# Optimization experiments

Measured on AMD Instinct MI355X. Metric: run time of the kernel, lower is better.

The kernel has to match this reference:

```python
import jax, jax.numpy as jnp
import numpy as np


def _lstm_dir(x, Wih, Whh, bih, bhh, reverse):
    # x: [B,T,D]; Wih: [4H,D]; Whh: [4H,H]; PyTorch gate order i,f,g,o
    if reverse:
        x = x[:, ::-1, :]
    H = Whh.shape[1]
    B = x.shape[0]
    # precompute input projection for all timesteps: [B,T,4H]
    xW = jnp.einsum('btd,gd->btg', x, Wih) + bih + bhh
    xW = jnp.swapaxes(xW, 0, 1)  # [T,B,4H]
    h0 = jnp.zeros((B, H), x.dtype)
    c0 = jnp.zeros((B, H), x.dtype)

    def step(carry, xt):
        h, c = carry
        g = xt + h @ Whh.T
        i, f, gg, o = jnp.split(g, 4, axis=-1)
        c = jax.nn.sigmoid(f) * c + jax.nn.sigmoid(i) * jnp.tanh(gg)
        h = jax.nn.sigmoid(o) * jnp.tanh(c)
        return (h, c), h

    _, ys = jax.lax.scan(step, (h0, c0), xW)
    ys = jnp.swapaxes(ys, 0, 1)  # [B,T,H]
    if reverse:
        ys = ys[:, ::-1, :]
    return ys


def _bilstm(x, Wih_f, Whh_f, bih_f, bhh_f, Wih_b, Whh_b, bih_b, bhh_b):
    yf = _lstm_dir(x, Wih_f, Whh_f, bih_f, bhh_f, False)
    yb = _lstm_dir(x, Wih_b, Whh_b, bih_b, bhh_b, True)
    return jnp.concatenate([yf, yb], axis=-1)


def setup_inputs() -> dict:
    key = jax.random.key(0)
    B, T, D = 1024, 512, 30
    H1, H2, DENSE, OUT = 96, 64, 32, 1
    ks = jax.random.split(key, 21)

    def U(k, shape, fan):
        bnd = 1.0 / np.sqrt(fan)
        return jax.random.uniform(k, shape, jnp.float32, -bnd, bnd)

    x = jax.random.normal(ks[0], (B, T, D), jnp.float32)
    inp = {'x': x}
    # layer 1 (input D -> H1), forward and backward directions
    inp['Wih1f'] = U(ks[1], (4 * H1, D), H1)
    inp['Whh1f'] = U(ks[2], (4 * H1, H1), H1)
    inp['bih1f'] = U(ks[3], (4 * H1,), H1)
    inp['bhh1f'] = U(ks[4], (4 * H1,), H1)
    inp['Wih1b'] = U(ks[5], (4 * H1, D), H1)
    inp['Whh1b'] = U(ks[6], (4 * H1, H1), H1)
    inp['bih1b'] = U(ks[7], (4 * H1,), H1)
    inp['bhh1b'] = U(ks[8], (4 * H1,), H1)
    # layer 2 (input 2*H1 -> H2)
    inp['Wih2f'] = U(ks[9], (4 * H2, 2 * H1), H2)
    inp['Whh2f'] = U(ks[10], (4 * H2, H2), H2)
    inp['bih2f'] = U(ks[11], (4 * H2,), H2)
    inp['bhh2f'] = U(ks[12], (4 * H2,), H2)
    inp['Wih2b'] = U(ks[13], (4 * H2, 2 * H1), H2)
    inp['Whh2b'] = U(ks[14], (4 * H2, H2), H2)
    inp['bih2b'] = U(ks[15], (4 * H2,), H2)
    inp['bhh2b'] = U(ks[16], (4 * H2,), H2)
    # dense head
    inp['W1'] = U(ks[17], (DENSE, 2 * H2), 2 * H2)
    inp['b1'] = U(ks[18], (DENSE,), 2 * H2)
    inp['W2'] = U(ks[19], (OUT, DENSE), DENSE)
    inp['b2'] = U(ks[20], (OUT,), DENSE)
    return inp


def reference(x, Wih1f, Whh1f, bih1f, bhh1f, Wih1b, Whh1b, bih1b, bhh1b,
              Wih2f, Whh2f, bih2f, bhh2f, Wih2b, Whh2b, bih2b, bhh2b,
              W1, b1, W2, b2):
    # dropout layers are identity in eval mode
    h1 = _bilstm(x, Wih1f, Whh1f, bih1f, bhh1f, Wih1b, Whh1b, bih1b, bhh1b)   # [B,T,192]
    h2 = _bilstm(h1, Wih2f, Whh2f, bih2f, bhh2f, Wih2b, Whh2b, bih2b, bhh2b)  # [B,T,128]
    last = h2[:, -1, :]                       # [B,128]
    d = jax.nn.relu(last @ W1.T + b1)         # [B,32]
    return d @ W2.T + b2                      # [B,1]
```

## Files before the change

kernel.cpp:

```cpp
#include <hip/hip_runtime.h>
#include <math.h>

#define B_  1024
#define T_  512
#define D_  30
#define H1_ 96
#define G1_ 384
#define H2_ 64
#define G2_ 256

__device__ float g_h1[(size_t)B_ * T_ * 192];
__device__ float g_h2f[(size_t)B_ * H2_];

__device__ __forceinline__ float fast_tanh(float v) {
  float a = fabsf(v);
  float e = __expf(-2.0f * a);
  float t = 1.0f - 2.0f * e / (1.0f + e);
  return v < 0.0f ? -t : t;
}
__device__ __forceinline__ float fast_sigmoid(float v) {
  return 0.5f + 0.5f * fast_tanh(0.5f * v);
}

#define FMAROW(a_, w_, v_)                                                    \
  a_ = fmaf(w_.x, v_.x, a_); a_ = fmaf(w_.y, v_.y, a_);                       \
  a_ = fmaf(w_.z, v_.z, a_); a_ = fmaf(w_.w, v_.w, a_);

#define BAR_LGKM() do {                                                       \
    asm volatile("s_waitcnt lgkmcnt(0)" ::: "memory");                        \
    __builtin_amdgcn_s_barrier();                                             \
    asm volatile("" ::: "memory");                                            \
  } while (0)

__global__ __launch_bounds__(768, 4)
void lstm1_kernel(const float* __restrict__ x,
                  const float* __restrict__ Wih_f, const float* __restrict__ Whh_f,
                  const float* __restrict__ bih_f, const float* __restrict__ bhh_f,
                  const float* __restrict__ Wih_b, const float* __restrict__ Whh_b,
                  const float* __restrict__ bih_b, const float* __restrict__ bhh_b)
{
  const int tid = threadIdx.x;
  const int dir = blockIdx.y;
  const int b0  = blockIdx.x * 8;

  const float* __restrict__ Wih = dir ? Wih_b : Wih_f;
  const float* __restrict__ Whh = dir ? Whh_b : Whh_f;
  const float* __restrict__ bih = dir ? bih_b : bih_f;
  const float* __restrict__ bhh = dir ? bhh_b : bhh_f;

  __shared__ __align__(16) float hx[8][128];
  __shared__ float gbuf[G1_ * 67];

  const int j = tid % 96;
  const int e = tid / 96;

  float4 wA0,wA1,wA2,wA3, wB0,wB1,wB2,wB3, wC0,wC1,wC2,wC3, wD0,wD1,wD2,wD3;
  if (e < 2) {
    const int k0 = e * 16;
#define LDXF(r_, kk) (((kk) < D_) ? Wih[(r_) * D_ + (kk)] : 0.0f)
#define LW4(d0,d1,d2,d3, r_) {                                                \
    d0 = make_float4(LDXF(r_,k0+ 0),LDXF(r_,k0+ 1),LDXF(r_,k0+ 2),LDXF(r_,k0+ 3)); \
    d1 = make_float4(LDXF(r_,k0+ 4),LDXF(r_,k0+ 5),LDXF(r_,k0+ 6),LDXF(r_,k0+ 7)); \
    d2 = make_float4(LDXF(r_,k0+ 8),LDXF(r_,k0+ 9),LDXF(r_,k0+10),LDXF(r_,k0+11)); \
    d3 = make_float4(LDXF(r_,k0+12),LDXF(r_,k0+13),LDXF(r_,k0+14),LDXF(r_,k0+15)); }
    LW4(wA0,wA1,wA2,wA3, j      )
    LW4(wB0,wB1,wB2,wB3, j +  96)
    LW4(wC0,wC1,wC2,wC3, j + 192)
    LW4(wD0,wD1,wD2,wD3, j + 288)
#undef LW4
#undef LDXF
  } else {
    const int c0 = e * 16 - 32;
    const float4* pA = (const float4*)(Whh + (j      ) * H1_ + c0);
    const float4* pB = (const float4*)(Whh + (j +  96) * H1_ + c0);
    const float4* pC = (const float4*)(Whh + (j + 192) * H1_ + c0);
    const float4* pD = (const float4*)(Whh + (j + 288) * H1_ + c0);
    wA0=pA[0]; wA1=pA[1]; wA2=pA[2]; wA3=pA[3];
    wB0=pB[0]; wB1=pB[1]; wB2=pB[2]; wB3=pB[3];
    wC0=pC[0]; wC1=pC[1]; wC2=pC[2]; wC3=pC[3];
    wD0=pD[0]; wD1=pD[1]; wD2=pD[2]; wD3=pD[3];
  }

  const float bias_i = bih[j      ] + bhh[j      ];
  const float bias_f = bih[j +  96] + bhh[j +  96];
  const float bias_g = bih[j + 192] + bhh[j + 192];
  const float bias_o = bih[j + 288] + bhh[j + 288];
  float c_state = 0.0f;

  for (int i = tid; i < 8 * 128; i += 768) (&hx[0][0])[i] = 0.0f;
  __syncthreads();
  const int xb = tid / 30;
  const int xd = tid - xb * 30;
  if (tid < 240) {
    const int t0 = dir ? (T_ - 1) : 0;
    hx[xb][xd] = x[((size_t)(b0 + xb) * T_ + t0) * D_ + xd];
  }
  __syncthreads();

  const int eoff = e * 4;
  const float4* hx4 = (const float4*)(&hx[0][0]);
  const int rA = (j      ) * 67 + e;
  const int rB = (j +  96) * 67 + e;
  const int rC = (j + 192) * 67 + e;
  const int rD = (j + 288) * 67 + e;
  const int ur = j * 67 + e * 8;

  for (int s = 0; s < T_; ++s) {
    const int t = dir ? (T_ - 1 - s) : s;
    float xn = 0.0f;
    if (tid < 240 && s + 1 < T_) {
      const int tn = dir ? (t - 1) : (t + 1);
      xn = x[((size_t)(b0 + xb) * T_ + tn) * D_ + xd];
    }
    float aA0=0.f,aA1=0.f,aA2=0.f,aA3=0.f,aA4=0.f,aA5=0.f,aA6=0.f,aA7=0.f;
    float aB0=0.f,aB1=0.f,aB2=0.f,aB3=0.f,aB4=0.f,aB5=0.f,aB6=0.f,aB7=0.f;
    float aC0=0.f,aC1=0.f,aC2=0.f,aC3=0.f,aC4=0.f,aC5=0.f,aC6=0.f,aC7=0.f;
    float aD0=0.f,aD1=0.f,aD2=0.f,aD3=0.f,aD4=0.f,aD5=0.f,aD6=0.f,aD7=0.f;
#define FB1(i) {                                                              \
    float4 v0 = hx4[0*32 + eoff + i]; float4 v1 = hx4[1*32 + eoff + i];       \
    float4 v2 = hx4[2*32 + eoff + i]; float4 v3 = hx4[3*32 + eoff + i];       \
    float4 v4 = hx4[4*32 + eoff + i]; float4 v5 = hx4[5*32 + eoff + i];       \
    float4 v6 = hx4[6*32 + eoff + i]; float4 v7 = hx4[7*32 + eoff + i];       \
    FMAROW(aA0, wA##i, v0) FMAROW(aB0, wB##i, v0)                             \
    FMAROW(aC0, wC##i, v0) FMAROW(aD0, wD##i, v0)                             \
    FMAROW(aA1, wA##i, v1) FMAROW(aB1, wB##i, v1)                             \
    FMAROW(aC1, wC##i, v1) FMAROW(aD1, wD##i, v1)                             \
    FMAROW(aA2, wA##i, v2) FMAROW(aB2, wB##i, v2)                             \
    FMAROW(aC2, wC##i, v2) FMAROW(aD2, wD##i, v2)                             \
    FMAROW(aA3, wA##i, v3) FMAROW(aB3, wB##i, v3)                             \
    FMAROW(aC3, wC##i, v3) FMAROW(aD3, wD##i, v3)                             \
    FMAROW(aA4, wA##i, v4) FMAROW(aB4, wB##i, v4)                             \
    FMAROW(aC4, wC##i, v4) FMAROW(aD4, wD##i, v4)                             \
    FMAROW(aA5, wA##i, v5) FMAROW(aB5, wB##i, v5)                             \
    FMAROW(aC5, wC##i, v5) FMAROW(aD5, wD##i, v5)                             \
    FMAROW(aA6, wA##i, v6) FMAROW(aB6, wB##i, v6)                             \
    FMAROW(aC6, wC##i, v6) FMAROW(aD6, wD##i, v6)                             \
    FMAROW(aA7, wA##i, v7) FMAROW(aB7, wB##i, v7)                             \
    FMAROW(aC7, wC##i, v7) FMAROW(aD7, wD##i, v7) }
    FB1(0) FB1(1) FB1(2) FB1(3)
#undef FB1
    {
      gbuf[rA+ 0]=aA0; gbuf[rA+ 8]=aA1; gbuf[rA+16]=aA2; gbuf[rA+24]=aA3;
      gbuf[rA+32]=aA4; gbuf[rA+40]=aA5; gbuf[rA+48]=aA6; gbuf[rA+56]=aA7;
      gbuf[rB+ 0]=aB0; gbuf[rB+ 8]=aB1; gbuf[rB+16]=aB2; gbuf[rB+24]=aB3;
      gbuf[rB+32]=aB4; gbuf[rB+40]=aB5; gbuf[rB+48]=aB6; gbuf[rB+56]=aB7;
      gbuf[rC+ 0]=aC0; gbuf[rC+ 8]=aC1; gbuf[rC+16]=aC2; gbuf[rC+24]=aC3;
      gbuf[rC+32]=aC4; gbuf[rC+40]=aC5; gbuf[rC+48]=aC6; gbuf[rC+56]=aC7;
      gbuf[rD+ 0]=aD0; gbuf[rD+ 8]=aD1; gbuf[rD+16]=aD2; gbuf[rD+24]=aD3;
      gbuf[rD+32]=aD4; gbuf[rD+40]=aD5; gbuf[rD+48]=aD6; gbuf[rD+56]=aD7;
    }
    BAR_LGKM();
    if (tid < 240 && s + 1 < T_) hx[xb][xd] = xn;
    {
      float gi = bias_i, gf = bias_f, gg = bias_g, go = bias_o;
#pragma unroll
      for (int c = 0; c < 8; ++c) {
        gi += gbuf[ur            + c];
        gf += gbuf[ur +  96 * 67 + c];
        gg += gbuf[ur + 192 * 67 + c];
        go += gbuf[ur + 288 * 67 + c];
      }
      float iv = fast_sigmoid(gi);
      float fv = fast_sigmoid(gf);
      float ov = fast_sigmoid(go);
      c_state = fv * c_state + iv * fast_tanh(gg);
      float h = ov * fast_tanh(c_state);
      hx[e][32 + j] = h;
      g_h1[((size_t)(b0 + e) * T_ + t) * 192 + dir * 96 + j] = h;
    }
    BAR_LGKM();
  }
}

__global__ __launch_bounds__(1024, 4)
void lstm2f_kernel(const float* __restrict__ Wih, const float* __restrict__ Whh,
                   const float* __restrict__ bih, const float* __restrict__ bhh)
{
  const int tid = threadIdx.x;
  const int b0  = blockIdx.x * 4;
  const int j   = tid & 63;
  const int e   = tid >> 6;

  __shared__ __align__(16) float hx[4][256];
  __shared__ float gbuf[G2_ * 67];

  const int k0 = e * 16;
  float4 wA0,wA1,wA2,wA3, wB0,wB1,wB2,wB3, wC0,wC1,wC2,wC3, wD0,wD1,wD2,wD3;
  if (e < 12) {
    const float4* pA = (const float4*)(Wih + (j      ) * 192 + k0);
    const float4* pB = (const float4*)(Wih + (j +  64) * 192 + k0);
    const float4* pC = (const float4*)(Wih + (j + 128) * 192 + k0);
    const float4* pD = (const float4*)(Wih + (j + 192) * 192 + k0);
    wA0=pA[0]; wA1=pA[1]; wA2=pA[2]; wA3=pA[3];
    wB0=pB[0]; wB1=pB[1]; wB2=pB[2]; wB3=pB[3];
    wC0=pC[0]; wC1=pC[1]; wC2=pC[2]; wC3=pC[3];
    wD0=pD[0]; wD1=pD[1]; wD2=pD[2]; wD3=pD[3];
  } else {
    const int c0 = k0 - 192;
    const float4* pA = (const float4*)(Whh + (j      ) * H2_ + c0);
    const float4* pB = (const float4*)(Whh + (j +  64) * H2_ + c0);
    const float4* pC = (const float4*)(Whh + (j + 128) * H2_ + c0);
    const float4* pD = (const float4*)(Whh + (j + 192) * H2_ + c0);
    wA0=pA[0]; wA1=pA[1]; wA2=pA[2]; wA3=pA[3];
    wB0=pB[0]; wB1=pB[1]; wB2=pB[2]; wB3=pB[3];
    wC0=pC[0]; wC1=pC[1]; wC2=pC[2]; wC3=pC[3];
    wD0=pD[0]; wD1=pD[1]; wD2=pD[2]; wD3=pD[3];
  }

  const int uj = tid & 63;
  const int ub = (tid >> 6) & 3;
  const float bias_i = bih[uj      ] + bhh[uj      ];
  const float bias_f = bih[uj +  64] + bhh[uj +  64];
  const float bias_g = bih[uj + 128] + bhh[uj + 128];
  const float bias_o = bih[uj + 192] + bhh[uj + 192];
  float c_state = 0.0f;

  for (int i = tid; i < 4 * 256; i += 1024) (&hx[0][0])[i] = 0.0f;
  __syncthreads();
  const int pb = tid / 96;
  const int pj = tid - pb * 96;
  if (tid < 384) {
    *(float2*)&hx[pb][pj * 2] =
        *(const float2*)&g_h1[((size_t)(b0 + pb) * T_ + 0) * 192 + pj * 2];
  }
  __syncthreads();

  const int eoff = e * 4;
  const float4* hx4 = (const float4*)(&hx[0][0]);
  const int rA = (j      ) * 67 + e;
  const int rB = (j +  64) * 67 + e;
  const int rC = (j + 128) * 67 + e;
  const int rD = (j + 192) * 67 + e;
  const int ur = uj * 67 + ub * 16;

  for (int s = 0; s < T_; ++s) {
    float2 pre = make_float2(0.0f, 0.0f);
    if (tid < 384 && s + 1 < T_) {
      pre = *(const float2*)&g_h1[((size_t)(b0 + pb) * T_ + (s + 1)) * 192 + pj * 2];
    }
    float aA0=0.f,aA1=0.f,aA2=0.f,aA3=0.f;
    float aB0=0.f,aB1=0.f,aB2=0.f,aB3=0.f;
    float aC0=0.f,aC1=0.f,aC2=0.f,aC3=0.f;
    float aD0=0.f,aD1=0.f,aD2=0.f,aD3=0.f;
#define FB2(i) {                                                              \
    float4 v0 = hx4[0*64 + eoff + i]; float4 v1 = hx4[1*64 + eoff + i];       \
    float4 v2 = hx4[2*64 + eoff + i]; float4 v3 = hx4[3*64 + eoff + i];       \
    FMAROW(aA0, wA##i, v0) FMAROW(aB0, wB##i, v0)                             \
    FMAROW(aC0, wC##i, v0) FMAROW(aD0, wD##i, v0)                             \
    FMAROW(aA1, wA##i, v1) FMAROW(aB1, wB##i, v1)                             \
    FMAROW(aC1, wC##i, v1) FMAROW(aD1, wD##i, v1)                             \
    FMAROW(aA2, wA##i, v2) FMAROW(aB2, wB##i, v2)                             \
    FMAROW(aC2, wC##i, v2) FMAROW(aD2, wD##i, v2)                             \
    FMAROW(aA3, wA##i, v3) FMAROW(aB3, wB##i, v3)                             \
    FMAROW(aC3, wC##i, v3) FMAROW(aD3, wD##i, v3) }
    FB2(0) FB2(1) FB2(2) FB2(3)
#undef FB2
    {
      gbuf[rA+ 0]=aA0; gbuf[rA+16]=aA1; gbuf[rA+32]=aA2; gbuf[rA+48]=aA3;
      gbuf[rB+ 0]=aB0; gbuf[rB+16]=aB1; gbuf[rB+32]=aB2; gbuf[rB+48]=aB3;
      gbuf[rC+ 0]=aC0; gbuf[rC+16]=aC1; gbuf[rC+32]=aC2; gbuf[rC+48]=aC3;
      gbuf[rD+ 0]=aD0; gbuf[rD+16]=aD1; gbuf[rD+32]=aD2; gbuf[rD+48]=aD3;
    }
    BAR_LGKM();
    if (tid < 384 && s + 1 < T_) *(float2*)&hx[pb][pj * 2] = pre;
    if (tid < 256) {
      float gi = bias_i, gf = bias_f, gg = bias_g, go = bias_o;
#pragma unroll
      for (int c = 0; c < 16; ++c) {
        gi += gbuf[ur            + c];
        gf += gbuf[ur +  64 * 67 + c];
        gg += gbuf[ur + 128 * 67 + c];
        go += gbuf[ur + 192 * 67 + c];
      }
      float iv = fast_sigmoid(gi), fv = fast_sigmoid(gf), ov = fast_sigmoid(go);
      c_state = fv * c_state + iv * fast_tanh(gg);
      float h = ov * fast_tanh(c_state);
      hx[ub][192 + uj] = h;
      if (s == T_ - 1) g_h2f[(b0 + ub) * H2_ + uj] = h;
    }
    BAR_LGKM();
  }
}

__global__ __launch_bounds__(256)
void tail_kernel(const float* __restrict__ Wih, const float* __restrict__ bih,
                 const float* __restrict__ bhh,
                 const float* __restrict__ W1, const float* __restrict__ b1,
                 const float* __restrict__ W2, const float* __restrict__ b2,
                 float* __restrict__ out)
{
  const int tid = threadIdx.x;
  const int b0  = blockIdx.x * 8;

  __shared__ __align__(16) float hl[8][192];
  __shared__ float gb[G2_ * 9];
  __shared__ __align__(16) float last[8][128];
  __shared__ float db[8][32];

  for (int i = tid; i < 8 * 96; i += 256) {
    int bb = i / 96, jj = i - (i / 96) * 96;
    *(float2*)&hl[bb][jj * 2] =
        *(const float2*)&g_h1[((size_t)(b0 + bb) * T_ + (T_ - 1)) * 192 + jj * 2];
  }
  for (int i = tid; i < 8 * 64; i += 256) {
    int bb = i >> 6, jj = i & 63;
    last[bb][jj] = g_h2f[(b0 + bb) * H2_ + jj];
  }
  __syncthreads();

  {
    const int gg_ = tid;
    const float* wr = Wih + gg_ * 192;
    const float bias = bih[gg_] + bhh[gg_];
    float acc[8];
#pragma unroll
    for (int b = 0; b < 8; ++b) acc[b] = bias;
#pragma unroll 4
    for (int qq = 0; qq < 48; ++qq) {
      float4 wv = *(const float4*)&wr[qq * 4];
#pragma unroll
      for (int b = 0; b < 8; ++b) {
        float4 v = *(const float4*)&hl[b][qq * 4];
        acc[b] = fmaf(wv.x, v.x, acc[b]);
        acc[b] = fmaf(wv.y, v.y, acc[b]);
        acc[b] = fmaf(wv.z, v.z, acc[b]);
        acc[b] = fmaf(wv.w, v.w, acc[b]);
      }
    }
#pragma unroll
    for (int b = 0; b < 8; ++b) gb[gg_ * 9 + b] = acc[b];
  }
  __syncthreads();

  for (int p = tid; p < 512; p += 256) {
    int jj = p & 63, bb = p >> 6;
    float gi = gb[(jj      ) * 9 + bb];
    float gg = gb[(jj + 128) * 9 + bb];
    float go = gb[(jj + 192) * 9 + bb];
    float c  = fast_sigmoid(gi) * fast_tanh(gg);
    float h  = fast_sigmoid(go) * fast_tanh(c);
    last[bb][64 + jj] = h;
  }
  __syncthreads();

  {
    int u = tid & 31, bb = tid >> 5;
    const float* wr1 = W1 + u * 128;
    float a = b1[u];
#pragma unroll
    for (int qq = 0; qq < 32; ++qq) {
      float4 wv = *(const float4*)&wr1[qq * 4];
      float4 v  = *(const float4*)&last[bb][qq * 4];
      a = fmaf(wv.x, v.x, a); a = fmaf(wv.y, v.y, a);
      a = fmaf(wv.z, v.z, a); a = fmaf(wv.w, v.w, a);
    }
    db[bb][u] = fmaxf(a, 0.0f);
  }
  __syncthreads();

  if (tid < 8) {
    float a = b2[0];
#pragma unroll
    for (int u2 = 0; u2 < 32; ++u2) a = fmaf(db[tid][u2], W2[u2], a);
    out[b0 + tid] = a;
  }
}

extern "C" void kernel_launch(void* const* d_in, const int* in_sizes, int n_in,
                              void* d_out, int out_size, void* d_ws, size_t ws_size,
                              hipStream_t stream)
{
  const float* x     = (const float*)d_in[0];
  const float* Wih1f = (const float*)d_in[1];
  const float* Whh1f = (const float*)d_in[2];
  const float* bih1f = (const float*)d_in[3];
  const float* bhh1f = (const float*)d_in[4];
  const float* Wih1b = (const float*)d_in[5];
  const float* Whh1b = (const float*)d_in[6];
  const float* bih1b = (const float*)d_in[7];
  const float* bhh1b = (const float*)d_in[8];
  const float* Wih2f = (const float*)d_in[9];
  const float* Whh2f = (const float*)d_in[10];
  const float* bih2f = (const float*)d_in[11];
  const float* bhh2f = (const float*)d_in[12];
  const float* Wih2b = (const float*)d_in[13];
  const float* bih2b = (const float*)d_in[15];
  const float* bhh2b = (const float*)d_in[16];
  const float* W1    = (const float*)d_in[17];
  const float* b1    = (const float*)d_in[18];
  const float* W2    = (const float*)d_in[19];
  const float* b2    = (const float*)d_in[20];

  (void)d_ws; (void)ws_size; (void)in_sizes; (void)n_in; (void)out_size;

  lstm1_kernel<<<dim3(128, 2), 768, 0, stream>>>(
      x, Wih1f, Whh1f, bih1f, bhh1f, Wih1b, Whh1b, bih1b, bhh1b);
  lstm2f_kernel<<<256, 1024, 0, stream>>>(
      Wih2f, Whh2f, bih2f, bhh2f);
  tail_kernel<<<128, 256, 0, stream>>>(
      Wih2b, bih2b, bhh2b, W1, b1, W2, b2, (float*)d_out);
}
```

Before: 2.967 ms.

## Remap LSTM threads so gate reduction stays within a wave; double-buffer hidden state

Both recurrent kernels now assign the K-slices of each hidden unit to consecutive lanes within one wavefront. Partial sums go to a per-wave float4 scratch and are reduced by the same wave without a block barrier. The hidden/input buffer is double-buffered in a padded, bank-friendly layout, which removes one of the two block-wide barriers per timestep. The cost is relying on implicit wave-level synchronisation for the scratch reduction, plus a more complex shared-memory indexing scheme.

After: 3.800 ms. +28.0%, slower.

```diff
diff --git a/kernel.cpp b/kernel.cpp
--- a/kernel.cpp
+++ b/kernel.cpp
@@ -48,11 +48,13 @@
   const float* __restrict__ bih = dir ? bih_b : bih_f;
   const float* __restrict__ bhh = dir ? bhh_b : bhh_f;
 
-  __shared__ __align__(16) float hx[8][128];
-  __shared__ float gbuf[G1_ * 67];
-
-  const int j = tid % 96;
-  const int e = tid / 96;
+  const int j  = tid >> 3;
+  const int e  = tid & 7;
+  const int wv = tid >> 6;
+  const int jl = j & 7;
+
+  __shared__ __align__(16) float hxs[2 * 1056];
+  __shared__ float4 scr4[12 * 520];
 
   float4 wA0,wA1,wA2,wA3, wB0,wB1,wB2,wB3, wC0,wC1,wC2,wC3, wD0,wD1,wD2,wD3;
   if (e < 2) {
@@ -87,87 +89,86 @@
   const float bias_o = bih[j + 288] + bhh[j + 288];
   float c_state = 0.0f;
 
-  for (int i = tid; i < 8 * 128; i += 768) (&hx[0][0])[i] = 0.0f;
+  for (int i = tid; i < 2 * 1056; i += 768) hxs[i] = 0.0f;
   __syncthreads();
   const int xb = tid / 30;
   const int xd = tid - xb * 30;
+  const int xoff = 132 * (xd >> 4) + 16 * xb + (xd & 15);
   if (tid < 240) {
     const int t0 = dir ? (T_ - 1) : 0;
-    hx[xb][xd] = x[((size_t)(b0 + xb) * T_ + t0) * D_ + xd];
-  }
-  __syncthreads();
-
-  const int eoff = e * 4;
-  const float4* hx4 = (const float4*)(&hx[0][0]);
-  const int rA = (j      ) * 67 + e;
-  const int rB = (j +  96) * 67 + e;
-  const int rC = (j + 192) * 67 + e;
-  const int rD = (j + 288) * 67 + e;
-  const int ur = j * 67 + e * 8;
+    hxs[xoff] = x[((size_t)(b0 + xb) * T_ + t0) * D_ + xd];
+  }
+  __syncthreads();
+
+  const int ef = 33 * e;
+  float4* scrw = scr4 + wv * 520 + jl * 65;
+  const int we8 = e * 8;
+  const int hoff = 132 * (2 + (j >> 4)) + 16 * e + ((32 + j) & 15);
+  float* __restrict__ gp = g_h1 + ((size_t)(b0 + e) * T_) * 192
+                                + (size_t)dir * 96 + j;
 
   for (int s = 0; s < T_; ++s) {
-    const int t = dir ? (T_ - 1 - s) : s;
+    const int t   = dir ? (T_ - 1 - s) : s;
+    const int cur = s & 1, nxt = cur ^ 1;
     float xn = 0.0f;
     if (tid < 240 && s + 1 < T_) {
       const int tn = dir ? (t - 1) : (t + 1);
       xn = x[((size_t)(b0 + xb) * T_ + tn) * D_ + xd];
     }
-    float aA0=0.f,aA1=0.f,aA2=0.f,aA3=0.f,aA4=0.f,aA5=0.f,aA6=0.f,aA7=0.f;
-    float aB0=0.f,aB1=0.f,aB2=0.f,aB3=0.f,aB4=0.f,aB5=0.f,aB6=0.f,aB7=0.f;
-    float aC0=0.f,aC1=0.f,aC2=0.f,aC3=0.f,aC4=0.f,aC5=0.f,aC6=0.f,aC7=0.f;
-    float aD0=0.f,aD1=0.f,aD2=0.f,aD3=0.f,aD4=0.f,aD5=0.f,aD6=0.f,aD7=0.f;
+    const float4* hb = (const float4*)(hxs + cur * 1056);
+    float aI0=0.f,aI1=0.f,aI2=0.f,aI3=0.f,aI4=0.f,aI5=0.f,aI6=0.f,aI7=0.f;
+    float aF0=0.f,aF1=0.f,aF2=0.f,aF3=0.f,aF4=0.f,aF5=0.f,aF6=0.f,aF7=0.f;
+    float aG0=0.f,aG1=0.f,aG2=0.f,aG3=0.f,aG4=0.f,aG5=0.f,aG6=0.f,aG7=0.f;
+    float aO0=0.f,aO1=0.f,aO2=0.f,aO3=0.f,aO4=0.f,aO5=0.f,aO6=0.f,aO7=0.f;
 #define FB1(i) {                                                              \
-    float4 v0 = hx4[0*32 + eoff + i]; float4 v1 = hx4[1*32 + eoff + i];       \
-    float4 v2 = hx4[2*32 + eoff + i]; float4 v3 = hx4[3*32 + eoff + i];       \
-    float4 v4 = hx4[4*32 + eoff + i]; float4 v5 = hx4[5*32 + eoff + i];       \
-    float4 v6 = hx4[6*32 + eoff + i]; float4 v7 = hx4[7*32 + eoff + i];       \
-    FMAROW(aA0, wA##i, v0) FMAROW(aB0, wB##i, v0)                             \
-    FMAROW(aC0, wC##i, v0) FMAROW(aD0, wD##i, v0)                             \
-    FMAROW(aA1, wA##i, v1) FMAROW(aB1, wB##i, v1)                             \
-    FMAROW(aC1, wC##i, v1) FMAROW(aD1, wD##i, v1)                             \
-    FMAROW(aA2, wA##i, v2) FMAROW(aB2, wB##i, v2)                             \
-    FMAROW(aC2, wC##i, v2) FMAROW(aD2, wD##i, v2)                             \
-    FMAROW(aA3, wA##i, v3) FMAROW(aB3, wB##i, v3)                             \
-    FMAROW(aC3, wC##i, v3) FMAROW(aD3, wD##i, v3)                             \
-    FMAROW(aA4, wA##i, v4) FMAROW(aB4, wB##i, v4)                             \
-    FMAROW(aC4, wC##i, v4) FMAROW(aD4, wD##i, v4)                             \
-    FMAROW(aA5, wA##i, v5) FMAROW(aB5, wB##i, v5)                             \
-    FMAROW(aC5, wC##i, v5) FMAROW(aD5, wD##i, v5)                             \
-    FMAROW(aA6, wA##i, v6) FMAROW(aB6, wB##i, v6)                             \
-    FMAROW(aC6, wC##i, v6) FMAROW(aD6, wD##i, v6)                             \
-    FMAROW(aA7, wA##i, v7) FMAROW(aB7, wB##i, v7)                             \
-    FMAROW(aC7, wC##i, v7) FMAROW(aD7, wD##i, v7) }
+    float4 v0 = hb[ef +  0 + i]; float4 v1 = hb[ef +  4 + i];                 \
+    float4 v2 = hb[ef +  8 + i]; float4 v3 = hb[ef + 12 + i];                 \
+    float4 v4 = hb[ef + 16 + i]; float4 v5 = hb[ef + 20 + i];                 \
+    float4 v6 = hb[ef + 24 + i]; float4 v7 = hb[ef + 28 + i];                 \
+    FMAROW(aI0, wA##i, v0) FMAROW(aF0, wB##i, v0)                             \
+    FMAROW(aG0, wC##i, v0) FMAROW(aO0, wD##i, v0)                             \
+    FMAROW(aI1, wA##i, v1) FMAROW(aF1, wB##i, v1)                             \
+    FMAROW(aG1, wC##i, v1) FMAROW(aO1, wD##i, v1)                             \
+    FMAROW(aI2, wA##i, v2) FMAROW(aF2, wB##i, v2)                             \
+    FMAROW(aG2, wC##i, v2) FMAROW(aO2, wD##i, v2)                             \
+    FMAROW(aI3, wA##i, v3) FMAROW(aF3, wB##i, v3)                             \
+    FMAROW(aG3, wC##i, v3) FMAROW(aO3, wD##i, v3)                             \
+    FMAROW(aI4, wA##i, v4) FMAROW(aF4, wB##i, v4)                             \
+    FMAROW(aG4, wC##i, v4) FMAROW(aO4, wD##i, v4)                             \
+    FMAROW(aI5, wA##i, v5) FMAROW(aF5, wB##i, v5)                             \
+    FMAROW(aG5, wC##i, v5) FMAROW(aO5, wD##i, v5)                             \
+    FMAROW(aI6, wA##i, v6) FMAROW(aF6, wB##i, v6)                             \
+    FMAROW(aG6, wC##i, v6) FMAROW(aO6, wD##i, v6)                             \
+    FMAROW(aI7, wA##i, v7) FMAROW(aF7, wB##i, v7)                             \
+    FMAROW(aG7, wC##i, v7) FMAROW(aO7, wD##i, v7) }
     FB1(0) FB1(1) FB1(2) FB1(3)
 #undef FB1
+    scrw[we8 + 0] = make_float4(aI0, aF0, aG0, aO0);
+    scrw[we8 + 1] = make_float4(aI1, aF1, aG1, aO1);
+    scrw[we8 + 2] = make_float4(aI2, aF2, aG2, aO2);
+    scrw[we8 + 3] = make_float4(aI3, aF3, aG3, aO3);
+    scrw[we8 + 4] = make_float4(aI4, aF4, aG4, aO4);
+    scrw[we8 + 5] = make_float4(aI5, aF5, aG5, aO5);
+    scrw[we8 + 6] = make_float4(aI6, aF6, aG6, aO6);
+    scrw[we8 + 7] = make_float4(aI7, aF7, aG7, aO7);
     {
-      gbuf[rA+ 0]=aA0; gbuf[rA+ 8]=aA1; gbuf[rA+16]=aA2; gbuf[rA+24]=aA3;
-      gbuf[rA+32]=aA4; gbuf[rA+40]=aA5; gbuf[rA+48]=aA6; gbuf[rA+56]=aA7;
-      gbuf[rB+ 0]=aB0; gbuf[rB+ 8]=aB1; gbuf[rB+16]=aB2; gbuf[rB+24]=aB3;
-      gbuf[rB+32]=aB4; gbuf[rB+40]=aB5; gbuf[rB+48]=aB6; gbuf[rB+56]=aB7;
-      gbuf[rC+ 0]=aC0; gbuf[rC+ 8]=aC1; gbuf[rC+16]=aC2; gbuf[rC+24]=aC3;
-      gbuf[rC+32]=aC4; gbuf[rC+40]=aC5; gbuf[rC+48]=aC6; gbuf[rC+56]=aC7;
-      gbuf[rD+ 0]=aD0; gbuf[rD+ 8]=aD1; gbuf[rD+16]=aD2; gbuf[rD+24]=aD3;
-      gbuf[rD+32]=aD4; gbuf[rD+40]=aD5; gbuf[rD+48]=aD6; gbuf[rD+56]=aD7;
-    }
-    BAR_LGKM();
-    if (tid < 240 && s + 1 < T_) hx[xb][xd] = xn;
-    {
-      float gi = bias_i, gf = bias_f, gg = bias_g, go = bias_o;
-#pragma unroll
-      for (int c = 0; c < 8; ++c) {
-        gi += gbuf[ur            + c];
-        gf += gbuf[ur +  96 * 67 + c];
-        gg += gbuf[ur + 192 * 67 + c];
-        go += gbuf[ur + 288 * 67 + c];
-      }
+      float4 r0 = scrw[ 0 + e], r1 = scrw[ 8 + e];
+      float4 r2 = scrw[16 + e], r3 = scrw[24 + e];
+      float4 r4 = scrw[32 + e], r5 = scrw[40 + e];
+      float4 r6 = scrw[48 + e], r7 = scrw[56 + e];
+      float gi = bias_i + r0.x + r1.x + r2.x + r3.x + r4.x + r5.x + r6.x + r7.x;
+      float gf = bias_f + r0.y + r1.y + r2.y + r3.y + r4.y + r5.y + r6.y + r7.y;
+      float gg = bias_g + r0.z + r1.z + r2.z + r3.z + r4.z + r5.z + r6.z + r7.z;
+      float go = bias_o + r0.w + r1.w + r2.w + r3.w + r4.w + r5.w + r6.w + r7.w;
       float iv = fast_sigmoid(gi);
       float fv = fast_sigmoid(gf);
       float ov = fast_sigmoid(go);
       c_state = fv * c_state + iv * fast_tanh(gg);
       float h = ov * fast_tanh(c_state);
-      hx[e][32 + j] = h;
-      g_h1[((size_t)(b0 + e) * T_ + t) * 192 + dir * 96 + j] = h;
-    }
+      hxs[nxt * 1056 + hoff] = h;
+      gp[(size_t)t * 192] = h;
+    }
+    if (tid < 240 && s + 1 < T_) hxs[nxt * 1056 + xoff] = xn;
     BAR_LGKM();
   }
 }
@@ -178,11 +179,13 @@
 {
   const int tid = threadIdx.x;
   const int b0  = blockIdx.x * 4;
-  const int j   = tid & 63;
-  const int e   = tid >> 6;
-
-  __shared__ __align__(16) float hx[4][256];
-  __shared__ float gbuf[G2_ * 67];
+  const int j   = tid >> 4;
+  const int e   = tid & 15;
+  const int wv  = tid >> 6;
+  const int jl  = j & 3;
+
+  __shared__ __align__(16) float hxs[2 * 1088];
+  __shared__ float4 scr4[16 * 260];
 
   const int k0 = e * 16;
   float4 wA0,wA1,wA2,wA3, wB0,wB1,wB2,wB3, wC0,wC1,wC2,wC3, wD0,wD1,wD2,wD3;
@@ -207,77 +210,70 @@
     wD0=pD[0]; wD1=pD[1]; wD2=pD[2]; wD3=pD[3];
   }
 
-  const int uj = tid & 63;
-  const int ub = (tid >> 6) & 3;
-  const float bias_i = bih[uj      ] + bhh[uj      ];
-  const float bias_f = bih[uj +  64] + bhh[uj +  64];
-  const float bias_g = bih[uj + 128] + bhh[uj + 128];
-  const float bias_o = bih[uj + 192] + bhh[uj + 192];
+  const float bias_i = bih[j      ] + bhh[j      ];
+  const float bias_f = bih[j +  64] + bhh[j +  64];
+  const float bias_g = bih[j + 128] + bhh[j + 128];
+  const float bias_o = bih[j + 192] + bhh[j + 192];
   float c_state = 0.0f;
 
-  for (int i = tid; i < 4 * 256; i += 1024) (&hx[0][0])[i] = 0.0f;
+  for (int i = tid; i < 2 * 1088; i += 1024) hxs[i] = 0.0f;
   __syncthreads();
   const int pb = tid / 96;
   const int pj = tid - pb * 96;
+  const int soff = 68 * ((2 * pj) >> 4) + 16 * pb + ((2 * pj) & 15);
   if (tid < 384) {
-    *(float2*)&hx[pb][pj * 2] =
+    *(float2*)&hxs[soff] =
         *(const float2*)&g_h1[((size_t)(b0 + pb) * T_ + 0) * 192 + pj * 2];
   }
   __syncthreads();
 
-  const int eoff = e * 4;
-  const float4* hx4 = (const float4*)(&hx[0][0]);
-  const int rA = (j      ) * 67 + e;
-  const int rB = (j +  64) * 67 + e;
-  const int rC = (j + 128) * 67 + e;
-  const int rD = (j + 192) * 67 + e;
-  const int ur = uj * 67 + ub * 16;
+  const int ef = 17 * e;
+  float4* scrw = scr4 + wv * 260 + jl * 65;
+  const int we4 = e * 4;
+  const int hoff = 68 * (12 + (j >> 4)) + 16 * e + (j & 15);
 
   for (int s = 0; s < T_; ++s) {
+    const int cur = s & 1, nxt = cur ^ 1;
     float2 pre = make_float2(0.0f, 0.0f);
     if (tid < 384 && s + 1 < T_) {
       pre = *(const float2*)&g_h1[((size_t)(b0 + pb) * T_ + (s + 1)) * 192 + pj * 2];
     }
-    float aA0=0.f,aA1=0.f,aA2=0.f,aA3=0.f;
-    float aB0=0.f,aB1=0.f,aB2=0.f,aB3=0.f;
-    float aC0=0.f,aC1=0.f,aC2=0.f,aC3=0.f;
-    float aD0=0.f,aD1=0.f,aD2=0.f,aD3=0.f;
+    const float4* hb = (const float4*)(hxs + cur * 1088);
+    float aI0=0.f,aI1=0.f,aI2=0.f,aI3=0.f;
+    float aF0=0.f,aF1=0.f,aF2=0.f,aF3=0.f;
+    float aG0=0.f,aG1=0.f,aG2=0.f,aG3=0.f;
+    float aO0=0.f,aO1=0.f,aO2=0.f,aO3=0.f;
 #define FB2(i) {                                                              \
-    float4 v0 = hx4[0*64 + eoff + i]; float4 v1 = hx4[1*64 + eoff + i];       \
-    float4 v2 = hx4[2*64 + eoff + i]; float4 v3 = hx4[3*64 + eoff + i];       \
-    FMAROW(aA0, wA##i, v0) FMAROW(aB0, wB##i, v0)                             \
-    FMAROW(aC0, wC##i, v0) FMAROW(aD0, wD##i, v0)                             \
-    FMAROW(aA1, wA##i, v1) FMAROW(aB1, wB##i, v1)                             \
-    FMAROW(aC1, wC##i, v1) FMAROW(aD1, wD##i, v1)                             \
-    FMAROW(aA2, wA##i, v2) FMAROW(aB2, wB##i, v2)                             \
-    FMAROW(aC2, wC##i, v2) FMAROW(aD2, wD##i, v2)                             \
-    FMAROW(aA3, wA##i, v3) FMAROW(aB3, wB##i, v3)                             \
-    FMAROW(aC3, wC##i, v3) FMAROW(aD3, wD##i, v3) }
+    float4 v0 = hb[ef + 0 + i]; float4 v1 = hb[ef + 4 + i];                   \
+    float4 v2 = hb[ef + 8 + i]; float4 v3 = hb[ef + 12 + i];                  \
+    FMAROW(aI0, wA##i, v0) FMAROW(aF0, wB##i, v0)                             \
+    FMAROW(aG0, wC##i, v0) FMAROW(aO0, wD##i, v0)                             \
+    FMAROW(aI1, wA##i, v1) FMAROW(aF1, wB##i, v1)                             \
+    FMAROW(aG1, wC##i, v1) FMAROW(aO1, wD##i, v1)                             \
+    FMAROW(aI2, wA##i, v2) FMAROW(aF2, wB##i, v2)                             \
+    FMAROW(aG2, wC##i, v2) FMAROW(aO2, wD##i, v2)                             \
+    FMAROW(aI3, wA##i, v3) FMAROW(aF3, wB##i, v3)                             \
+    FMAROW(aG3, wC##i, v3) FMAROW(aO3, wD##i, v3) }
     FB2(0) FB2(1) FB2(2) FB2(3)
 #undef FB2
-    {
-      gbuf[rA+ 0]=aA0; gbuf[rA+16]=aA1; gbuf[rA+32]=aA2; gbuf[rA+48]=aA3;
-      gbuf[rB+ 0]=aB0; gbuf[rB+16]=aB1; gbuf[rB+32]=aB2; gbuf[rB+48]=aB3;
-      gbuf[rC+ 0]=aC0; gbuf[rC+16]=aC1; gbuf[rC+32]=aC2; gbuf[rC+48]=aC3;
-      gbuf[rD+ 0]=aD0; gbuf[rD+16]=aD1; gbuf[rD+32]=aD2; gbuf[rD+48]=aD3;
-    }
-    BAR_LGKM();
-    if (tid < 384 && s + 1 < T_) *(float2*)&hx[pb][pj * 2] = pre;
-    if (tid < 256) {
+    scrw[we4 + 0] = make_float4(aI0, aF0, aG0, aO0);
+    scrw[we4 + 1] = make_float4(aI1, aF1, aG1, aO1);
+    scrw[we4 + 2] = make_float4(aI2, aF2, aG2, aO2);
+    scrw[we4 + 3] = make_float4(aI3, aF3, aG3, aO3);
+    if (e < 4) {
       float gi = bias_i, gf = bias_f, gg = bias_g, go = bias_o;
 #pragma unroll
-      for (int c = 0; c < 16; ++c) {
-        gi += gbuf[ur            + c];
-        gf += gbuf[ur +  64 * 67 + c];
-        gg += gbuf[ur + 128 * 67 + c];
-        go += gbuf[ur + 192 * 67 + c];
+      for (int ee = 0; ee < 16; ++ee) {
+        float4 r = scrw[ee * 4 + e];
+        gi += r.x; gf += r.y; gg += r.z; go += r.w;
       }
       float iv = fast_sigmoid(gi), fv = fast_sigmoid(gf), ov = fast_sigmoid(go);
       c_state = fv * c_state + iv * fast_tanh(gg);
       float h = ov * fast_tanh(c_state);
-      hx[ub][192 + uj] = h;
-      if (s == T_ - 1) g_h2f[(b0 + ub) * H2_ + uj] = h;
-    }
+      hxs[nxt * 1088 + hoff] = h;
+      if (s == T_ - 1) g_h2f[(b0 + e) * H2_ + j] = h;
+    }
+    if (tid < 384 && s + 1 < T_) *(float2*)&hxs[nxt * 1088 + soff] = pre;
     BAR_LGKM();
   }
 }
```
